# Kernel optimization log

Hardware: AMD Instinct MI355X
Metric: run time of the kernel (lower is better)

## Reference

```python
import jax, jax.numpy as jnp
import numpy as np

D_MODEL = 2048
NUM_HEADS = 32
HEAD_DIM = D_MODEL // NUM_HEADS  # 64
ROPE_BASE = 10000.0


def _rope_cos_sin(seq_len, head_dim, dtype):
    inv_freq = 1.0 / (ROPE_BASE ** (jnp.arange(0, head_dim, 2, dtype=jnp.float32) / head_dim))
    freqs = jnp.arange(seq_len, dtype=jnp.float32)[:, None] * inv_freq[None, :]  # (S, Dh/2)
    emb = jnp.concatenate([freqs, freqs], axis=-1)  # (S, Dh)
    return emb.astype(dtype), jnp.cos(emb).astype(dtype), jnp.sin(emb).astype(dtype)


def _rotate_half(x):
    x1, x2 = jnp.split(x, 2, axis=-1)
    return jnp.concatenate([-x2, x1], axis=-1)


def setup_inputs() -> dict:
    key = jax.random.key(0)
    k1, k2, k3, k4 = jax.random.split(key, 4)
    B, S, D = 1, 2048, D_MODEL
    x = jax.random.normal(k1, (B, S, D), dtype=jnp.float32)
    Wqkv = jax.random.normal(k2, (3 * D, D), dtype=jnp.float32) * 0.02
    Wo = jax.random.normal(k3, (D, D), dtype=jnp.float32) * 0.02
    gate = jax.random.normal(k4, (D,), dtype=jnp.float32) * 0.1
    return {"x": x, "Wqkv": Wqkv, "Wo": Wo, "gate": gate}


def reference(x, Wqkv, Wo, gate):
    B, S, D = x.shape
    H, Dh = NUM_HEADS, HEAD_DIM
    residual = x

    # fused QKV projection (torch Linear: y = x @ W.T)
    qkv = jnp.einsum('bsd,ed->bse', x, Wqkv).reshape(B, S, 3, H, Dh)
    q, k, v = qkv[:, :, 0], qkv[:, :, 1], qkv[:, :, 2]  # each (B, S, H, Dh)

    # RoPE
    _, cos, sin = _rope_cos_sin(S, Dh, x.dtype)
    cos = cos[None, :, None, :]  # (1, S, 1, Dh)
    sin = sin[None, :, None, :]
    q = q * cos + _rotate_half(q) * sin
    k = k * cos + _rotate_half(k) * sin

    # causal SDPA
    scale = 1.0 / np.sqrt(Dh)
    scores = jnp.einsum('bqhd,bkhd->bhqk', q, k) * scale  # (B, H, S, S)
    causal = jnp.tril(jnp.ones((S, S), dtype=bool))
    scores = jnp.where(causal[None, None], scores, jnp.finfo(scores.dtype).min)
    probs = jax.nn.softmax(scores, axis=-1)
    attn = jnp.einsum('bhqk,bkhd->bqhd', probs, v).reshape(B, S, D)

    out = jnp.einsum('bsd,ed->bse', attn, Wo)
    # HeoGate: learned per-channel gated residual (assumption; see notes)
    return residual + gate * out
```

## Files before the change

kernel.cpp:

```cpp
#include <hip/hip_runtime.h>
#include <hip/hip_bf16.h>
#include <cstdint>
#include <cstddef>

typedef __hip_bfloat16 bf16;
typedef short short8 __attribute__((ext_vector_type(8)));
typedef float f32x4 __attribute__((ext_vector_type(4)));

#define S_LEN 2048
#define DMODEL 2048
#define NQKV 6144
#define NHEADS 32
#define HDIM 64
#define ROPE_L2 0.4152410118609203f

__device__ __forceinline__ void async_copy16(const bf16* g, bf16* l) {
  __builtin_amdgcn_global_load_lds(
      (const __attribute__((address_space(1))) void*)g,
      (__attribute__((address_space(3))) void*)l, 16, 0, 0);
}

__device__ __forceinline__ f32x4 mfma_bf16(short8 a, short8 b, f32x4 c) {
  return __builtin_amdgcn_mfma_f32_16x16x32_bf16(a, b, c, 0, 0, 0);
}

__global__ __launch_bounds__(256) void cvt3_kernel(const float* __restrict__ sx,
                                                   bf16* __restrict__ dx,
                                                   const float* __restrict__ sw,
                                                   bf16* __restrict__ dw,
                                                   const float* __restrict__ so,
                                                   bf16* __restrict__ dov) {
  int i = blockIdx.x * 256 + threadIdx.x;
  const float* s;
  bf16* d;
  if (i < 1048576) {
    s = sx; d = dx;
  } else if (i < 4194304) {
    s = sw; d = dw; i -= 1048576;
  } else {
    s = so; d = dov; i -= 4194304;
  }
  const float4 v = ((const float4*)s)[i];
  union { bf16 h[4]; ushort4 u; } tmp;
  tmp.h[0] = __float2bfloat16(v.x);
  tmp.h[1] = __float2bfloat16(v.y);
  tmp.h[2] = __float2bfloat16(v.z);
  tmp.h[3] = __float2bfloat16(v.w);
  ((ushort4*)d)[i] = tmp.u;
}

#define QKV_NT 32
#define QBAR() do { __builtin_amdgcn_s_barrier(); __builtin_amdgcn_sched_barrier(0); } while (0)
#define WAITV(n) asm volatile("s_waitcnt vmcnt(" #n ")" ::: "memory")
#define LGKM0() do { asm volatile("s_waitcnt lgkmcnt(0)" ::: "memory"); \
                     __builtin_amdgcn_sched_barrier(0); } while (0)

__global__ __launch_bounds__(256, 2) void gemm_qkv(const bf16* __restrict__ A,
                                                   const bf16* __restrict__ W,
                                                   bf16* __restrict__ q_ws,
                                                   bf16* __restrict__ k_ws,
                                                   bf16* __restrict__ v_ws) {
  __shared__ bf16 smem[32768];
  const int tid = threadIdx.x;
  const int wave = tid >> 6, lane = tid & 63;
  const int wm = wave >> 1, wn = wave & 1;
  const int m0 = blockIdx.y * 128, n0 = blockIdx.x * 128;
  const int srow = tid >> 2;
  const int swc = (((tid & 3) ^ ((tid >> 3) & 3)) * 8);
  const int fr = lane & 15, fq = lane >> 4;
  const int rdc = ((fq ^ ((fr >> 1) & 3)) * 8);

  const bf16* Asrc = A + (size_t)(m0 + srow) * DMODEL + swc;
  const bf16* Bsrc = W + (size_t)(n0 + srow) * DMODEL + swc;

  auto stage = [&](int t_, int bufe_) {
#pragma unroll
    for (int kk = 0; kk < 2; ++kk) {
      const int ko = t_ * 64 + kk * 32;
      async_copy16(Asrc + ko, &smem[bufe_ + kk * 4096 + wave * 512]);
      async_copy16(Asrc + (size_t)64 * DMODEL + ko,
                   &smem[bufe_ + kk * 4096 + 2048 + wave * 512]);
      async_copy16(Bsrc + ko, &smem[bufe_ + 8192 + kk * 4096 + wave * 512]);
      async_copy16(Bsrc + (size_t)64 * DMODEL + ko,
                   &smem[bufe_ + 8192 + kk * 4096 + 2048 + wave * 512]);
    }
  };

  const f32x4 zero = {0.f, 0.f, 0.f, 0.f};
  f32x4 acc[4][4];
#pragma unroll
  for (int i = 0; i < 4; ++i)
#pragma unroll
    for (int j = 0; j < 4; ++j) acc[i][j] = zero;
  short8 a0[4], a1[4], b0[4], b1[4];

  stage(0, 0);
  stage(1, 16384);
  WAITV(8);
  QBAR();

#pragma unroll 2
  for (int t = 0; t < QKV_NT; ++t) {
    const int bc = (t & 1) * 16384;
#pragma unroll
    for (int mi = 0; mi < 4; ++mi) {
      const int ro = (wm * 64 + mi * 16 + fr) * 32 + rdc;
      a0[mi] = *(const short8*)&smem[bc + ro];
      a1[mi] = *(const short8*)&smem[bc + 4096 + ro];
    }
#pragma unroll
    for (int n = 0; n < 4; ++n) {
      const int ro = (wn * 64 + n * 16 + fr) * 32 + rdc;
      b0[n] = *(const short8*)&smem[bc + 8192 + ro];
      b1[n] = *(const short8*)&smem[bc + 12288 + ro];
    }
    LGKM0();
    QBAR();
    if (t + 2 < QKV_NT) stage(t + 2, bc);
    __builtin_amdgcn_s_setprio(1);
#pragma unroll
    for (int mi = 0; mi < 4; ++mi)
#pragma unroll
      for (int n = 0; n < 4; ++n)
        acc[mi][n] = mfma_bf16(a0[mi], b0[n], acc[mi][n]);
#pragma unroll
    for (int mi = 0; mi < 4; ++mi)
#pragma unroll
      for (int n = 0; n < 4; ++n)
        acc[mi][n] = mfma_bf16(a1[mi], b1[n], acc[mi][n]);
    __builtin_amdgcn_s_setprio(0);
    if (t + 2 < QKV_NT)      { WAITV(8); }
    else if (t + 1 < QKV_NT) { WAITV(0); }
    QBAR();
  }

  const int colb = n0 + wn * 64;
  const int sect = colb >> 11;
  const int h = (colb & 2047) >> 6;
  const int col = fr, rq = fq * 4;

  if (sect < 2) {
    bf16* dst = ((sect == 0) ? q_ws : k_ws) + (size_t)h * S_LEN * HDIM;
    bf16* rep = smem + wave * 1152;
    const float f0 = exp2f(-(float)col * ROPE_L2);
    const float f1 = exp2f(-(float)(16 + col) * ROPE_L2);
    __syncthreads();
    for (int m = 0; m < 4; ++m) {
      const int base_s = m0 + wm * 64 + m * 16;
#pragma unroll
      for (int jl = 0; jl < 2; ++jl) {
        const int dh = jl * 16 + col;
        const float fr_ = (jl == 0) ? f0 : f1;
#pragma unroll
        for (int r = 0; r < 4; ++r) {
          const int srw = base_s + rq + r;
          float sn, cs;
          __sincosf((float)srw * fr_, &sn, &cs);
          const float xl = acc[m][jl][r], xh = acc[m][jl + 2][r];
          rep[(rq + r) * 72 + dh]      = __float2bfloat16(xl * cs - xh * sn);
          rep[(rq + r) * 72 + dh + 32] = __float2bfloat16(xh * cs + xl * sn);
        }
      }
#pragma unroll
      for (int p = 0; p < 2; ++p) {
        const int rr = p * 8 + (lane >> 3), ch = lane & 7;
        const uint4 vv = *(const uint4*)&rep[rr * 72 + ch * 8];
        *(uint4*)&dst[(size_t)(base_s + rr) * HDIM + ch * 8] = vv;
      }
    }
  } else {
    bf16* dst = v_ws + (size_t)h * HDIM * S_LEN;
    for (int j = 0; j < 4; ++j) {
      const int dh = j * 16 + col;
      for (int m = 0; m < 4; ++m) {
        const int s0 = m0 + wm * 64 + m * 16 + rq;
        union { bf16 hx[4]; uint2 u; } vk;
#pragma unroll
        for (int r = 0; r < 4; ++r) vk.hx[r] = __float2bfloat16(acc[m][j][r]);
        *(uint2*)&dst[(size_t)dh * S_LEN + s0] = vk.u;
      }
    }
  }
}

__global__ __launch_bounds__(256) void attn_kernel(const bf16* __restrict__ q_ws,
                                                   const bf16* __restrict__ k_ws,
                                                   const bf16* __restrict__ vt_ws,
                                                   bf16* __restrict__ attn_out) {
  const int bid = blockIdx.x;
  const int qt = 15 - (bid >> 5);
  const int h = bid & 31;

  const int tid = threadIdx.x, wave = tid >> 6, lane = tid & 63;
  const int col = lane & 15, fq = lane >> 4;
  const int qbase = qt * 128 + wave * 32;

  __shared__ bf16 Ks[2][64 * 64];
  __shared__ bf16 Vs[2][64 * 64];
  __shared__ bf16 Pl[4][32 * 72];
  bf16* pl = Pl[wave];

  const bf16* qh = q_ws + (size_t)h * S_LEN * HDIM;
  const bf16* kh = k_ws + (size_t)h * S_LEN * HDIM;
  const bf16* vh = vt_ws + (size_t)h * HDIM * S_LEN;

  const int srow = lane >> 3;
  const int slot = lane & 7;
  const int schunk = slot ^ srow;

  auto stage = [&](int kt, int buf) {
    const int k0 = kt * 64;
#pragma unroll
    for (int j = 0; j < 2; ++j) {
      const int r8 = (wave * 2 + j) * 8;
      async_copy16(kh + (size_t)(k0 + r8 + srow) * HDIM + schunk * 8,
                   &Ks[buf][r8 * 64]);
      async_copy16(vh + (size_t)(r8 + srow) * S_LEN + k0 + schunk * 8,
                   &Vs[buf][r8 * 64]);
    }
  };

  short8 qf[2][2];
#pragma unroll
  for (int g = 0; g < 2; ++g)
#pragma unroll
    for (int ks = 0; ks < 2; ++ks)
      qf[g][ks] = *(const short8*)&qh[(size_t)(qbase + g * 16 + col) * HDIM +
                                      ks * 32 + fq * 8];

  const f32x4 zero = {0.f, 0.f, 0.f, 0.f};
  f32x4 o_acc[2][4];
#pragma unroll
  for (int g = 0; g < 2; ++g)
#pragma unroll
    for (int n = 0; n < 4; ++n) o_acc[g][n] = zero;
  float m_i[2] = {-1e30f, -1e30f}, l_i[2] = {0.f, 0.f};

  stage(0, 0);

  const int lastk = 2 * qt + 1;
  for (int kt = 0; kt <= lastk; ++kt) {
    const int buf = kt & 1;
    const int k0 = kt * 64;
    __syncthreads();
    if (kt < lastk) stage(kt + 1, buf ^ 1);

    short8 kf[8];
#pragma unroll
    for (int n = 0; n < 4; ++n) {
      const int row = n * 16 + col;
#pragma unroll
      for (int ks = 0; ks < 2; ++ks)
        kf[n * 2 + ks] =
            *(const short8*)&Ks[buf][row * 64 + (((ks * 4 + fq) ^ (row & 7)) * 8)];
    }
    f32x4 s_acc[2][4];
#pragma unroll
    for (int g = 0; g < 2; ++g)
#pragma unroll
      for (int n = 0; n < 4; ++n) s_acc[g][n] = zero;
#pragma unroll
    for (int g = 0; g < 2; ++g)
#pragma unroll
      for (int n = 0; n < 4; ++n)
#pragma unroll
        for (int ks = 0; ks < 2; ++ks)
          s_acc[g][n] = mfma_bf16(kf[n * 2 + ks], qf[g][ks], s_acc[g][n]);

    short8 vf[8];
#pragma unroll
    for (int n = 0; n < 4; ++n) {
      const int row = n * 16 + col;
#pragma unroll
      for (int ks = 0; ks < 2; ++ks)
        vf[n * 2 + ks] =
            *(const short8*)&Vs[buf][row * 64 + (((ks * 4 + fq) ^ (row & 7)) * 8)];
    }

    if (k0 + 63 > qbase) {
#pragma unroll
      for (int g = 0; g < 2; ++g) {
        const int qg = qbase + g * 16 + col;
#pragma unroll
        for (int n = 0; n < 4; ++n)
#pragma unroll
          for (int r = 0; r < 4; ++r)
            if (k0 + n * 16 + fq * 4 + r > qg) s_acc[g][n][r] = -1e30f;
      }
    }

#pragma unroll
    for (int g = 0; g < 2; ++g) {
      float vmax = -1e30f;
#pragma unroll
      for (int n = 0; n < 4; ++n)
#pragma unroll
        for (int r = 0; r < 4; ++r) vmax = fmaxf(vmax, s_acc[g][n][r]);
      vmax = fmaxf(vmax, __shfl_xor(vmax, 16, 64));
      vmax = fmaxf(vmax, __shfl_xor(vmax, 32, 64));

      if (!__all(vmax - m_i[g] <= 8.0f)) {
        const float mnew = fmaxf(m_i[g], vmax);
        const float alpha = __expf((m_i[g] - mnew) * 0.125f);
        l_i[g] *= alpha;
#pragma unroll
        for (int n = 0; n < 4; ++n)
#pragma unroll
          for (int r = 0; r < 4; ++r) o_acc[g][n][r] *= alpha;
        m_i[g] = mnew;
      }

      float rs = 0.f;
#pragma unroll
      for (int n = 0; n < 4; ++n)
#pragma unroll
        for (int r = 0; r < 4; ++r) {
          const float p = __expf((s_acc[g][n][r] - m_i[g]) * 0.125f);
          s_acc[g][n][r] = p;
          rs += p;
        }
      rs += __shfl_xor(rs, 16, 64);
      rs += __shfl_xor(rs, 32, 64);
      l_i[g] += rs;

#pragma unroll
      for (int n = 0; n < 4; ++n) {
        union { bf16 hx[4]; uint2 u; } pk;
#pragma unroll
        for (int r = 0; r < 4; ++r) pk.hx[r] = __float2bfloat16(s_acc[g][n][r]);
        *(uint2*)&pl[(g * 16 + col) * 72 + n * 16 + fq * 4] = pk.u;
      }
    }

    short8 pa[2][2];
#pragma unroll
    for (int g = 0; g < 2; ++g)
#pragma unroll
      for (int ks = 0; ks < 2; ++ks)
        pa[g][ks] = *(const short8*)&pl[(g * 16 + col) * 72 + ks * 32 + fq * 8];

#pragma unroll
    for (int g = 0; g < 2; ++g)
#pragma unroll
      for (int n = 0; n < 4; ++n)
#pragma unroll
        for (int ks = 0; ks < 2; ++ks)
          o_acc[g][n] = mfma_bf16(vf[n * 2 + ks], pa[g][ks], o_acc[g][n]);
  }

#pragma unroll
  for (int g = 0; g < 2; ++g) {
    const float inv = 1.0f / l_i[g];
    const int qg = qbase + g * 16 + col;
#pragma unroll
    for (int n = 0; n < 4; ++n) {
#pragma unroll
      for (int r = 0; r < 4; ++r) o_acc[g][n][r] *= inv;
      union { bf16 hx[4]; uint2 u; } ok;
#pragma unroll
      for (int r = 0; r < 4; ++r) ok.hx[r] = __float2bfloat16(o_acc[g][n][r]);
      *(uint2*)&attn_out[(size_t)qg * DMODEL + h * HDIM + n * 16 + fq * 4] = ok.u;
    }
  }
}

__global__ __launch_bounds__(256) void gemm_out(const bf16* __restrict__ A,
                                                const bf16* __restrict__ W,
                                                const float* __restrict__ xres,
                                                const float* __restrict__ gate,
                                                float* __restrict__ out) {
  constexpr int K = DMODEL;
  constexpr int NT = K / 32;
  __shared__ bf16 As[3][64 * 32];
  __shared__ bf16 Bs[3][128 * 32];
  const int tid = threadIdx.x;
  const int wave = tid >> 6, lane = tid & 63;
  const int m0 = blockIdx.y * 64, n0 = blockIdx.x * 128;
  const int sr = lane >> 2;
  const int swc = (((lane & 3) ^ ((lane >> 3) & 3)) * 8);
  const int fr = lane & 15, fq = lane >> 4;
  const int rdc = ((fq ^ ((fr >> 1) & 3)) * 8);

  auto stage = [&](int t_, int s_) {
    async_copy16(A + (size_t)(m0 + wave * 16 + sr) * K + t_ * 32 + swc,
                 &As[s_][(wave * 16) * 32]);
#pragma unroll
    for (int j = 0; j < 2; ++j)
      async_copy16(W + (size_t)(n0 + wave * 32 + j * 16 + sr) * K + t_ * 32 + swc,
                   &Bs[s_][(wave * 32 + j * 16) * 32]);
  };

  const f32x4 zero = {0.f, 0.f, 0.f, 0.f};
  f32x4 acc[4][2];
  for (int i = 0; i < 4; ++i)
    for (int j = 0; j < 2; ++j) acc[i][j] = zero;

  stage(0, 0);
  stage(1, 1);
  WAITV(3);
  QBAR();

  for (int t = 0; t < NT; ++t) {
    const int s = t % 3;
    short8 a[4], b[2];
#pragma unroll
    for (int i = 0; i < 4; ++i)
      a[i] = *(const short8*)&As[s][(i * 16 + fr) * 32 + rdc];
#pragma unroll
    for (int j = 0; j < 2; ++j)
      b[j] = *(const short8*)&Bs[s][(wave * 32 + j * 16 + fr) * 32 + rdc];
    LGKM0();
    QBAR();
    if (t + 2 < NT) stage(t + 2, (t + 2) % 3);
#pragma unroll
    for (int i = 0; i < 4; ++i)
#pragma unroll
      for (int j = 0; j < 2; ++j)
        acc[i][j] = mfma_bf16(a[i], b[j], acc[i][j]);
    if (t + 1 < NT) {
      if (t + 2 < NT) { WAITV(3); }
      else            { WAITV(0); }
      QBAR();
    }
  }

  const int col = fr, rq = fq * 4;
  for (int j = 0; j < 2; ++j) {
    const int cc = n0 + wave * 32 + j * 16 + col;
    const float g = gate[cc];
    for (int i = 0; i < 4; ++i) {
      const int base_row = m0 + i * 16 + rq;
      for (int r = 0; r < 4; ++r) {
        const size_t idx = (size_t)(base_row + r) * DMODEL + cc;
        out[idx] = xres[idx] + g * acc[i][j][r];
      }
    }
  }
}

extern "C" void kernel_launch(void* const* d_in, const int* in_sizes, int n_in,
                              void* d_out, int out_size, void* d_ws, size_t ws_size,
                              hipStream_t stream) {
  const float* x    = (const float*)d_in[0];
  const float* Wqkv = (const float*)d_in[1];
  const float* Wo   = (const float*)d_in[2];
  const float* gate = (const float*)d_in[3];
  float* out = (float*)d_out;

  char* ws = (char*)d_ws;
  const size_t MB = 1024 * 1024;
  bf16* xb      = (bf16*)(ws);
  bf16* wqkvb   = (bf16*)(ws + 8 * MB);
  bf16* wob     = (bf16*)(ws + 32 * MB);
  bf16* q_ws    = (bf16*)(ws + 40 * MB);
  bf16* k_ws    = (bf16*)(ws + 48 * MB);
  bf16* v_ws    = (bf16*)(ws + 56 * MB);
  bf16* attn_ws = (bf16*)(ws);

  cvt3_kernel<<<dim3(20480), 256, 0, stream>>>(x, xb, Wqkv, wqkvb, Wo, wob);

  gemm_qkv<<<dim3(NQKV / 128, S_LEN / 128), 256, 0, stream>>>(xb, wqkvb, q_ws, k_ws, v_ws);
  attn_kernel<<<dim3(512), 256, 0, stream>>>(q_ws, k_ws, v_ws, attn_ws);
  gemm_out<<<dim3(DMODEL / 128, DMODEL / 64), 256, 0, stream>>>(attn_ws, wob, x, gate, out);
}
```

Measured before the change: 259.2 us.

## Pair causal query tiles per block with 8 waves and prescale Q for exp2

The attention kernel now launches 256 blocks of 512 threads. Each block handles two query tiles in sequence (15-pr, then pr) to even out causal work across blocks, and each wave owns 16 query rows instead of 32. Q is prescaled during the RoPE epilogue by 1/sqrt(Dh)*log2(e), so the softmax uses exp2f directly with no per-element multiply. In exchange, each wave now does fewer MFMAs per K/V tile load, there are twice as many barriers per pass, and only 256 blocks run, which lowers available parallelism on a GPU with many CUs.

```diff
diff --git a/kernel.cpp b/kernel.cpp
--- a/kernel.cpp
+++ b/kernel.cpp
@@ -13,6 +13,7 @@
 #define NHEADS 32
 #define HDIM 64
 #define ROPE_L2 0.4152410118609203f
+#define Q_PRESCALE 0.18033688011112042f
 
 __device__ __forceinline__ void async_copy16(const bf16* g, bf16* l) {
   __builtin_amdgcn_global_load_lds(
@@ -142,6 +143,7 @@
   if (sect < 2) {
     bf16* dst = ((sect == 0) ? q_ws : k_ws) + (size_t)h * S_LEN * HDIM;
     bf16* rep = smem + wave * 1152;
+    const float qs = (sect == 0) ? Q_PRESCALE : 1.0f;
     const float f0 = exp2f(-(float)col * ROPE_L2);
     const float f1 = exp2f(-(float)(16 + col) * ROPE_L2);
     __syncthreads();
@@ -157,8 +159,8 @@
           float sn, cs;
           __sincosf((float)srw * fr_, &sn, &cs);
           const float xl = acc[m][jl][r], xh = acc[m][jl + 2][r];
-          rep[(rq + r) * 72 + dh]      = __float2bfloat16(xl * cs - xh * sn);
-          rep[(rq + r) * 72 + dh + 32] = __float2bfloat16(xh * cs + xl * sn);
+          rep[(rq + r) * 72 + dh]      = __float2bfloat16((xl * cs - xh * sn) * qs);
+          rep[(rq + r) * 72 + dh + 32] = __float2bfloat16((xh * cs + xl * sn) * qs);
         }
       }
 #pragma unroll
@@ -183,21 +185,20 @@
   }
 }
 
-__global__ __launch_bounds__(256) void attn_kernel(const bf16* __restrict__ q_ws,
+__global__ __launch_bounds__(512) void attn_kernel(const bf16* __restrict__ q_ws,
                                                    const bf16* __restrict__ k_ws,
                                                    const bf16* __restrict__ vt_ws,
                                                    bf16* __restrict__ attn_out) {
   const int bid = blockIdx.x;
-  const int qt = 15 - (bid >> 5);
+  const int pr = bid >> 5;
   const int h = bid & 31;
 
   const int tid = threadIdx.x, wave = tid >> 6, lane = tid & 63;
   const int col = lane & 15, fq = lane >> 4;
-  const int qbase = qt * 128 + wave * 32;
 
   __shared__ bf16 Ks[2][64 * 64];
   __shared__ bf16 Vs[2][64 * 64];
-  __shared__ bf16 Pl[4][32 * 72];
+  __shared__ bf16 Pl[8][16 * 72];
   bf16* pl = Pl[wave];
 
   const bf16* qh = q_ws + (size_t)h * S_LEN * HDIM;
@@ -210,104 +211,87 @@
 
   auto stage = [&](int kt, int buf) {
     const int k0 = kt * 64;
-#pragma unroll
-    for (int j = 0; j < 2; ++j) {
-      const int r8 = (wave * 2 + j) * 8;
-      async_copy16(kh + (size_t)(k0 + r8 + srow) * HDIM + schunk * 8,
-                   &Ks[buf][r8 * 64]);
-      async_copy16(vh + (size_t)(r8 + srow) * S_LEN + k0 + schunk * 8,
-                   &Vs[buf][r8 * 64]);
-    }
+    const int r8 = wave * 8;
+    async_copy16(kh + (size_t)(k0 + r8 + srow) * HDIM + schunk * 8,
+                 &Ks[buf][r8 * 64]);
+    async_copy16(vh + (size_t)(r8 + srow) * S_LEN + k0 + schunk * 8,
+                 &Vs[buf][r8 * 64]);
   };
 
-  short8 qf[2][2];
-#pragma unroll
-  for (int g = 0; g < 2; ++g)
+  const f32x4 zero = {0.f, 0.f, 0.f, 0.f};
+
+  for (int pass = 0; pass < 2; ++pass) {
+    const int qt = (pass == 0) ? (15 - pr) : pr;
+    const int q_glob = qt * 128 + wave * 16 + col;
+
+    short8 qf[2];
 #pragma unroll
     for (int ks = 0; ks < 2; ++ks)
-      qf[g][ks] = *(const short8*)&qh[(size_t)(qbase + g * 16 + col) * HDIM +
-                                      ks * 32 + fq * 8];
-
-  const f32x4 zero = {0.f, 0.f, 0.f, 0.f};
-  f32x4 o_acc[2][4];
-#pragma unroll
-  for (int g = 0; g < 2; ++g)
-#pragma unroll
-    for (int n = 0; n < 4; ++n) o_acc[g][n] = zero;
-  float m_i[2] = {-1e30f, -1e30f}, l_i[2] = {0.f, 0.f};
-
-  stage(0, 0);
-
-  const int lastk = 2 * qt + 1;
-  for (int kt = 0; kt <= lastk; ++kt) {
-    const int buf = kt & 1;
-    const int k0 = kt * 64;
-    __syncthreads();
-    if (kt < lastk) stage(kt + 1, buf ^ 1);
-
-    short8 kf[8];
-#pragma unroll
-    for (int n = 0; n < 4; ++n) {
-      const int row = n * 16 + col;
-#pragma unroll
-      for (int ks = 0; ks < 2; ++ks)
-        kf[n * 2 + ks] =
-            *(const short8*)&Ks[buf][row * 64 + (((ks * 4 + fq) ^ (row & 7)) * 8)];
-    }
-    f32x4 s_acc[2][4];
-#pragma unroll
-    for (int g = 0; g < 2; ++g)
-#pragma unroll
-      for (int n = 0; n < 4; ++n) s_acc[g][n] = zero;
-#pragma unroll
-    for (int g = 0; g < 2; ++g)
-#pragma unroll
-      for (int n = 0; n < 4; ++n)
+      qf[ks] = *(const short8*)&qh[(size_t)q_glob * HDIM + ks * 32 + fq * 8];
+
+    f32x4 o_acc[4] = {zero, zero, zero, zero};
+    float m_i = -1e30f, l_i = 0.f;
+
+    stage(0, 0);
+
+    const int lastk = 2 * qt + 1;
+    for (int kt = 0; kt <= lastk; ++kt) {
+      const int buf = kt & 1;
+      const int k0 = kt * 64;
+      __syncthreads();
+      if (kt < lastk) stage(kt + 1, buf ^ 1);
+
+      short8 kf[8];
+#pragma unroll
+      for (int n = 0; n < 4; ++n) {
+        const int row = n * 16 + col;
 #pragma unroll
         for (int ks = 0; ks < 2; ++ks)
-          s_acc[g][n] = mfma_bf16(kf[n * 2 + ks], qf[g][ks], s_acc[g][n]);
-
-    short8 vf[8];
-#pragma unroll
-    for (int n = 0; n < 4; ++n) {
-      const int row = n * 16 + col;
-#pragma unroll
-      for (int ks = 0; ks < 2; ++ks)
-        vf[n * 2 + ks] =
-            *(const short8*)&Vs[buf][row * 64 + (((ks * 4 + fq) ^ (row & 7)) * 8)];
-    }
-
-    if (k0 + 63 > qbase) {
-#pragma unroll
-      for (int g = 0; g < 2; ++g) {
-        const int qg = qbase + g * 16 + col;
+          kf[n * 2 + ks] =
+              *(const short8*)&Ks[buf][row * 64 + (((ks * 4 + fq) ^ (row & 7)) * 8)];
+      }
+      f32x4 s_acc[4] = {zero, zero, zero, zero};
+#pragma unroll
+      for (int n = 0; n < 4; ++n)
+#pragma unroll
+        for (int ks = 0; ks < 2; ++ks)
+          s_acc[n] = mfma_bf16(kf[n * 2 + ks], qf[ks], s_acc[n]);
+
+      short8 vf[8];
+#pragma unroll
+      for (int n = 0; n < 4; ++n) {
+        const int row = n * 16 + col;
+#pragma unroll
+        for (int ks = 0; ks < 2; ++ks)
+          vf[n * 2 + ks] =
+              *(const short8*)&Vs[buf][row * 64 + (((ks * 4 + fq) ^ (row & 7)) * 8)];
+      }
+
+      if (k0 + 63 > qt * 128 + wave * 16) {
 #pragma unroll
         for (int n = 0; n < 4; ++n)
 #pragma unroll
           for (int r = 0; r < 4; ++r)
-            if (k0 + n * 16 + fq * 4 + r > qg) s_acc[g][n][r] = -1e30f;
-      }
-    }
-
-#pragma unroll
-    for (int g = 0; g < 2; ++g) {
+            if (k0 + n * 16 + fq * 4 + r > q_glob) s_acc[n][r] = -1e30f;
+      }
+
       float vmax = -1e30f;
 #pragma unroll
       for (int n = 0; n < 4; ++n)
 #pragma unroll
-        for (int r = 0; r < 4; ++r) vmax = fmaxf(vmax, s_acc[g][n][r]);
+        for (int r = 0; r < 4; ++r) vmax = fmaxf(vmax, s_acc[n][r]);
       vmax = fmaxf(vmax, __shfl_xor(vmax, 16, 64));
       vmax = fmaxf(vmax, __shfl_xor(vmax, 32, 64));
 
-      if (!__all(vmax - m_i[g] <= 8.0f)) {
-        const float mnew = fmaxf(m_i[g], vmax);
-        const float alpha = __expf((m_i[g] - mnew) * 0.125f);
-        l_i[g] *= alpha;
+      if (!__all(vmax - m_i <= 8.0f)) {
+        const float mnew = fmaxf(m_i, vmax);
+        const float alpha = exp2f(m_i - mnew);
+        l_i *= alpha;
 #pragma unroll
         for (int n = 0; n < 4; ++n)
 #pragma unroll
-          for (int r = 0; r < 4; ++r) o_acc[g][n][r] *= alpha;
-        m_i[g] = mnew;
+          for (int r = 0; r < 4; ++r) o_acc[n][r] *= alpha;
+        m_i = mnew;
       }
 
       float rs = 0.f;
@@ -315,51 +299,42 @@
       for (int n = 0; n < 4; ++n)
 #pragma unroll
         for (int r = 0; r < 4; ++r) {
-          const float p = __expf((s_acc[g][n][r] - m_i[g]) * 0.125f);
-          s_acc[g][n][r] = p;
+          const float p = exp2f(s_acc[n][r] - m_i);
+          s_acc[n][r] = p;
           rs += p;
         }
       rs += __shfl_xor(rs, 16, 64);
       rs += __shfl_xor(rs, 32, 64);
-      l_i[g] += rs;
+      l_i += rs;
 
 #pragma unroll
       for (int n = 0; n < 4; ++n) {
         union { bf16 hx[4]; uint2 u; } pk;
 #pragma unroll
-        for (int r = 0; r < 4; ++r) pk.hx[r] = __float2bfloat16(s_acc[g][n][r]);
-        *(uint2*)&pl[(g * 16 + col) * 72 + n * 16 + fq * 4] = pk.u;
-      }
-    }
-
-    short8 pa[2][2];
-#pragma unroll
-    for (int g = 0; g < 2; ++g)
+        for (int r = 0; r < 4; ++r) pk.hx[r] = __float2bfloat16(s_acc[n][r]);
+        *(uint2*)&pl[col * 72 + n * 16 + fq * 4] = pk.u;
+      }
+      short8 pa[2];
 #pragma unroll
       for (int ks = 0; ks < 2; ++ks)
-        pa[g][ks] = *(const short8*)&pl[(g * 16 + col) * 72 + ks * 32 + fq * 8];
-
-#pragma unroll
-    for (int g = 0; g < 2; ++g)
+        pa[ks] = *(const short8*)&pl[col * 72 + ks * 32 + fq * 8];
+
 #pragma unroll
       for (int n = 0; n < 4; ++n)
 #pragma unroll
         for (int ks = 0; ks < 2; ++ks)
-          o_acc[g][n] = mfma_bf16(vf[n * 2 + ks], pa[g][ks], o_acc[g][n]);
-  }
-
-#pragma unroll
-  for (int g = 0; g < 2; ++g) {
-    const float inv = 1.0f / l_i[g];
-    const int qg = qbase + g * 16 + col;
+          o_acc[n] = mfma_bf16(vf[n * 2 + ks], pa[ks], o_acc[n]);
+    }
+
+    const float inv = 1.0f / l_i;
 #pragma unroll
     for (int n = 0; n < 4; ++n) {
 #pragma unroll
-      for (int r = 0; r < 4; ++r) o_acc[g][n][r] *= inv;
+      for (int r = 0; r < 4; ++r) o_acc[n][r] *= inv;
       union { bf16 hx[4]; uint2 u; } ok;
 #pragma unroll
-      for (int r = 0; r < 4; ++r) ok.hx[r] = __float2bfloat16(o_acc[g][n][r]);
-      *(uint2*)&attn_out[(size_t)qg * DMODEL + h * HDIM + n * 16 + fq * 4] = ok.u;
+      for (int r = 0; r < 4; ++r) ok.hx[r] = __float2bfloat16(o_acc[n][r]);
+      *(uint2*)&attn_out[(size_t)q_glob * DMODEL + h * HDIM + n * 16 + fq * 4] = ok.u;
     }
   }
 }
@@ -460,6 +435,6 @@
   cvt3_kernel<<<dim3(20480), 256, 0, stream>>>(x, xb, Wqkv, wqkvb, Wo, wob);
 
   gemm_qkv<<<dim3(NQKV / 128, S_LEN / 128), 256, 0, stream>>>(xb, wqkvb, q_ws, k_ws, v_ws);
-  attn_kernel<<<dim3(512), 256, 0, stream>>>(q_ws, k_ws, v_ws, attn_ws);
+  attn_kernel<<<dim3(256), 512, 0, stream>>>(q_ws, k_ws, v_ws, attn_ws);
   gemm_out<<<dim3(DMODEL / 128, DMODEL / 64), 256, 0, stream>>>(attn_ws, wob, x, gate, out);
 }
```

Measured after the change: 253.2 us. 1.02x faster.
